# Kernel optimization log

Measured on AMD Instinct MI355X. Metric: run time of the kernel, lower is better.

The kernel has to match this reference:

```python
import jax, jax.numpy as jnp
import numpy as np

GRID_SIZE = 8
POS_LAMBDA = 250.0
POS_MARGIN = 1.0
NEG_MARGIN = 0.2


def setup_inputs() -> dict:
    key = jax.random.key(0)
    k1, k2, k3, k4 = jax.random.split(key, 4)
    N, C, Hr, Wr = 8, 128, 30, 40
    H, W = Hr * GRID_SIZE, Wr * GRID_SIZE
    des1 = jax.random.normal(k1, (N, C, Hr, Wr), jnp.float32)
    des2 = jax.random.normal(k2, (N, C, Hr, Wr), jnp.float32)
    # near-identity homography so the positive-pair mask s is non-trivial
    homo = jnp.eye(3, dtype=jnp.float32) + 0.001 * jax.random.normal(k3, (3, 3), jnp.float32)
    mask = (jax.random.uniform(k4, (N, 1, H, W)) > 0.05).astype(jnp.float32)
    return {"des1": des1, "des2": des2, "homo": homo, "mask": mask}


def reference(des1, des2, homo, mask):
    n, c, hr, wr = des1.shape
    gs = GRID_SIZE

    # coordinate grid of cell centers in full-res pixel coords: (x, y)
    ys, xs = jnp.meshgrid(jnp.arange(hr), jnp.arange(wr), indexing='ij')
    grid = jnp.stack([xs, ys], axis=-1).astype(homo.dtype) * gs + gs // 2  # Hr,Wr,2
    grid = jnp.broadcast_to(grid, (n, hr, wr, 2))

    # warp grid by homography
    gh = jnp.concatenate([grid, jnp.ones((n, hr, wr, 1), homo.dtype)], axis=-1)  # N,Hr,Wr,3
    wg = jnp.einsum('nhwk,jk->nhwj', gh, homo)
    w_grid = wg[..., :2] / wg[..., 2:3]  # N,Hr,Wr,2

    # pairwise distance between grid cells of img1 and warped cells of img2
    diff = grid[:, :, :, None, None, :] - w_grid[:, None, None, :, :, :]  # N,Hr,Wr,Hr,Wr,2
    grid_dist = jnp.sqrt(jnp.sum(diff * diff, axis=-1))                   # N,Hr,Wr,Hr,Wr
    s = (grid_dist <= gs - 0.5).astype(des1.dtype)

    # dense descriptor cross-correlation (contraction over channels)
    dot_des = jnp.einsum('ncij,nckl->nijkl', des1, des2)  # N,Hr,Wr,Hr,Wr

    pos_dist = jnp.maximum(POS_MARGIN - dot_des, 0.0)
    neg_dist = jnp.maximum(dot_des - NEG_MARGIN, 0.0)
    loss = POS_LAMBDA * s * pos_dist + (1.0 - s) * neg_dist

    # space_to_depth(mask, gs).prod(dim=1)
    m = mask.reshape(n, 1, hr, gs, wr, gs)
    r_mask = jnp.prod(m, axis=(1, 3, 5))            # N,Hr,Wr
    r_mask5 = r_mask.reshape(n, 1, 1, hr, wr)

    norm = hr * wr * jnp.sum(r_mask5)
    loss = jnp.sum(loss * r_mask5) / norm
    return (loss, s, dot_des, r_mask5[:, 0])  # r_mask squeezed -> N,1,Hr,Wr
```

## Files before the change

kernel.cpp:

```cpp
#include <hip/hip_runtime.h>
#include <hip/hip_bf16.h>

#define HRr 30
#define WRr 40
#define MM 1200
#define CC 128
#define NB 8
#define GS 8

constexpr int PT = 19;
constexpr int TILE_SH = 16 * 64 * 8;
constexpr int NTASK = 4800;

typedef __attribute__((ext_vector_type(8))) short bf16x8;
typedef __attribute__((ext_vector_type(4))) float f32x4;

__device__ inline short f2bf(float f) {
    union { float f; unsigned u; } v; v.f = f;
    unsigned r = v.u + 0x7FFFu + ((v.u >> 16) & 1u);
    return (short)(r >> 16);
}

__global__ __launch_bounds__(256) void convert_prep_kernel(const float* __restrict__ des1,
                                                           const float* __restrict__ des2,
                                                           const float* __restrict__ homo,
                                                           const float* __restrict__ mask,
                                                           short* __restrict__ wsA,
                                                           short* __restrict__ wsB,
                                                           float2* __restrict__ wgrid,
                                                           float* __restrict__ out_rmask,
                                                           float* __restrict__ ws_rmask) {
    const int t     = threadIdx.x;
    const int ptile = blockIdx.x;
    const int n     = blockIdx.z;

    if (blockIdx.y == 0) {
        const int gid = (blockIdx.z * gridDim.x + blockIdx.x) * 256 + t;
        if (gid < MM) {
            int k = gid / WRr, l = gid % WRr;
            float x = (float)(l * GS + GS / 2);
            float y = (float)(k * GS + GS / 2);
            float nx = homo[0] * x + homo[1] * y + homo[2];
            float ny = homo[3] * x + homo[4] * y + homo[5];
            float dn = homo[6] * x + homo[7] * y + homo[8];
            wgrid[gid] = make_float2(nx / dn, ny / dn);
        }
        if (gid < NB * MM) {
            int nn = gid / MM;
            int rem = gid % MM;
            int k = rem / WRr, l = rem % WRr;
            const float* mp = mask + (size_t)nn * (240 * 320) + (size_t)(k * GS) * 320 + l * GS;
            float prod = 1.f;
            #pragma unroll
            for (int yy = 0; yy < GS; ++yy) {
                float4 a = *reinterpret_cast<const float4*>(&mp[yy * 320]);
                float4 b = *reinterpret_cast<const float4*>(&mp[yy * 320 + 4]);
                prod *= a.x * a.y * a.z * a.w * b.x * b.y * b.z * b.w;
            }
            out_rmask[gid] = prod;
            ws_rmask[gid]  = prod;
        }
    }

    const int lane = t & 63;
    const int g    = t >> 6;
    const int p    = ptile * 64 + lane;
    const int kr   = blockIdx.y * 2 + (g >> 1);
    const int kb   = kr * 8;
    const int isB  = g & 1;

    const float* src = (isB ? des2 : des1) + (size_t)n * CC * MM;
    short* dst = (isB ? wsB : wsA) + (size_t)(n * PT + ptile) * TILE_SH;

    bf16x8 wv;
    #pragma unroll
    for (int i = 0; i < 8; ++i) {
        float v = (p < MM) ? src[(size_t)(kb + i) * MM + p] : 0.f;
        wv[i] = f2bf(v);
    }
    const int rb = lane >> 4, lc = lane & 15;
    const int ks = kr >> 2, lrk = kr & 3;
    const size_t off = (size_t)(((ks * 4 + rb) * 64) + lrk * 16 + lc) * 8;
    *reinterpret_cast<bf16x8*>(&dst[off]) = wv;
}

__global__ __launch_bounds__(256) void main_kernel(const short* __restrict__ wsA,
                                                   const short* __restrict__ wsB,
                                                   const float2* __restrict__ wgrid,
                                                   const float* __restrict__ rmask,
                                                   float* __restrict__ out_s,
                                                   float* __restrict__ out_dot,
                                                   float* __restrict__ partials) {
    __shared__ float Ds[16 * 164];
    __shared__ float red[4];

    const int f   = blockIdx.x;
    const int n   = f & 7;
    const int idx = f >> 3;
    const int strip  = idx >> 3;
    const int e      = idx & 7;
    const int p0     = strip * 16;
    const int fbase  = e * 9 + (e < 3 ? e : 3);
    const int nf     = (e < 3) ? 10 : 9;
    const int cbase  = fbase * 16;
    const int W      = nf * 16;

    const int t    = threadIdx.x;
    const int lane = t & 63;
    const int w    = t >> 6;
    const int lr   = lane >> 4, lc = lane & 15;

    const short* An  = wsA + (size_t)(n * PT + (p0 >> 6)) * TILE_SH;
    const int    rbA = (p0 >> 4) & 3;
    bf16x8 af[4];
    #pragma unroll
    for (int ks = 0; ks < 4; ++ks)
        af[ks] = *reinterpret_cast<const bf16x8*>(&An[(size_t)(((ks * 4 + rbA) * 64) + lane) * 8]);

    const short* Bn = wsB + (size_t)n * PT * TILE_SH;
    const float* rm = rmask + n * MM;

    for (int i = w; i < nf; i += 4) {
        const int g = fbase + i;
        const short* Bt = Bn + (size_t)(g >> 2) * TILE_SH;
        const int rbB = g & 3;
        f32x4 acc = {0.f, 0.f, 0.f, 0.f};
        #pragma unroll
        for (int ks = 0; ks < 4; ++ks) {
            bf16x8 bfr = *reinterpret_cast<const bf16x8*>(
                &Bt[(size_t)(((ks * 4 + rbB) * 64) + lane) * 8]);
            acc = __builtin_amdgcn_mfma_f32_16x16x32_bf16(af[ks], bfr, acc, 0, 0, 0);
        }
        #pragma unroll
        for (int r = 0; r < 4; ++r)
            Ds[(lr * 4 + r) * 164 + 1 + i * 16 + lc] = acc[r];
    }
    __syncthreads();

    const int row = t >> 4;
    const int l16 = t & 15;
    const int p   = p0 + row;
    const float gx = (float)((p % WRr) * GS + GS / 2);
    const float gy = (float)((p / WRr) * GS + GS / 2);
    const size_t rowbase = (size_t)(n * MM + p) * MM;
    const float* dsr = &Ds[row * 164 + 1];
    const int h = 31 - 16 * (p & 1);
    const int cAl = (((h - cbase) % 32) + 32) % 32;

    float a0 = 0.f, a1 = 0.f, a2 = 0.f, a3 = 0.f;

    for (int c = l16; c < cAl; c += 16) {
        const float dot = dsr[c];
        const int q = cbase + c;
        const float2 wg = wgrid[q];
        const float dx = gx - wg.x, dy = gy - wg.y;
        const float d2 = dx * dx + dy * dy;
        const float s = (d2 <= 56.25f) ? 1.f : 0.f;
        const float le = 250.f * s * fmaxf(1.f - dot, 0.f) + (1.f - s) * fmaxf(dot - 0.2f, 0.f);
        a0 += le * rm[q];
        out_dot[rowbase + q] = dot;
        out_s[rowbase + q] = s;
    }
    const int nl = (W - cAl) >> 5;
    const int s4 = nl << 3;
    const int ts = cAl + (nl << 5);
    for (int k = 0;; ++k) {
        const int jj = l16 + (k << 4);
        if (jj >= s4) break;
        const int c = cAl + (jj << 2);
        const int q = cbase + c;
        const f32x4 dv = *reinterpret_cast<const f32x4*>(&dsr[c]);
        f32x4 sv;
        {
            const float2 wg0 = wgrid[q];
            const float2 wg1 = wgrid[q + 1];
            const float2 wg2 = wgrid[q + 2];
            const float2 wg3 = wgrid[q + 3];
            const float dx0 = gx - wg0.x, dy0 = gy - wg0.y;
            const float dx1 = gx - wg1.x, dy1 = gy - wg1.y;
            const float dx2 = gx - wg2.x, dy2 = gy - wg2.y;
            const float dx3 = gx - wg3.x, dy3 = gy - wg3.y;
            sv[0] = (dx0 * dx0 + dy0 * dy0 <= 56.25f) ? 1.f : 0.f;
            sv[1] = (dx1 * dx1 + dy1 * dy1 <= 56.25f) ? 1.f : 0.f;
            sv[2] = (dx2 * dx2 + dy2 * dy2 <= 56.25f) ? 1.f : 0.f;
            sv[3] = (dx3 * dx3 + dy3 * dy3 <= 56.25f) ? 1.f : 0.f;
        }
        const float le0 = 250.f * sv[0] * fmaxf(1.f - dv[0], 0.f) + (1.f - sv[0]) * fmaxf(dv[0] - 0.2f, 0.f);
        const float le1 = 250.f * sv[1] * fmaxf(1.f - dv[1], 0.f) + (1.f - sv[1]) * fmaxf(dv[1] - 0.2f, 0.f);
        const float le2 = 250.f * sv[2] * fmaxf(1.f - dv[2], 0.f) + (1.f - sv[2]) * fmaxf(dv[2] - 0.2f, 0.f);
        const float le3 = 250.f * sv[3] * fmaxf(1.f - dv[3], 0.f) + (1.f - sv[3]) * fmaxf(dv[3] - 0.2f, 0.f);
        a0 += le0 * rm[q];
        a1 += le1 * rm[q + 1];
        a2 += le2 * rm[q + 2];
        a3 += le3 * rm[q + 3];
        *reinterpret_cast<f32x4*>(&out_dot[rowbase + q]) = dv;
        *reinterpret_cast<f32x4*>(&out_s[rowbase + q]) = sv;
    }
    for (int c = ts + l16; c < W; c += 16) {
        const float dot = dsr[c];
        const int q = cbase + c;
        const float2 wg = wgrid[q];
        const float dx = gx - wg.x, dy = gy - wg.y;
        const float d2 = dx * dx + dy * dy;
        const float s = (d2 <= 56.25f) ? 1.f : 0.f;
        const float le = 250.f * s * fmaxf(1.f - dot, 0.f) + (1.f - s) * fmaxf(dot - 0.2f, 0.f);
        a1 += le * rm[q];
        out_dot[rowbase + q] = dot;
        out_s[rowbase + q] = s;
    }

    float lsum = (a0 + a1) + (a2 + a3);

    #pragma unroll
    for (int off = 32; off > 0; off >>= 1)
        lsum += __shfl_xor(lsum, off, 64);
    if (lane == 0) red[w] = lsum;
    __syncthreads();
    if (t == 0)
        partials[f] = (red[0] + red[1]) + (red[2] + red[3]);
}

__global__ __launch_bounds__(1024) void final_kernel(const float* __restrict__ partials,
                                                     const float* __restrict__ rmask,
                                                     float* __restrict__ out_loss) {
    __shared__ float r1[16], r2[16];
    const int t = threadIdx.x;
    const int lane = t & 63;
    const int w = t >> 6;

    float s1 = 0.f, s2 = 0.f;
    for (int i = t; i < NTASK; i += 1024) s1 += partials[i];
    for (int i = t; i < NB * MM; i += 1024) s2 += rmask[i];
    #pragma unroll
    for (int off = 32; off > 0; off >>= 1) {
        s1 += __shfl_xor(s1, off, 64);
        s2 += __shfl_xor(s2, off, 64);
    }
    if (lane == 0) { r1[w] = s1; r2[w] = s2; }
    __syncthreads();
    if (t == 0) {
        float total = 0.f, rsum = 0.f;
        #pragma unroll
        for (int i = 0; i < 16; ++i) { total += r1[i]; rsum += r2[i]; }
        out_loss[0] = total / ((float)MM * rsum);
    }
}

extern "C" void kernel_launch(void* const* d_in, const int* in_sizes, int n_in,
                              void* d_out, int out_size, void* d_ws, size_t ws_size,
                              hipStream_t stream) {
    const float* des1 = (const float*)d_in[0];
    const float* des2 = (const float*)d_in[1];
    const float* homo = (const float*)d_in[2];
    const float* mask = (const float*)d_in[3];

    float* out      = (float*)d_out;
    float* out_loss = out;
    float* out_s    = out + 1;
    float* out_dot  = out + 1 + (size_t)NB * MM * MM;
    float* out_rm   = out + 1 + 2 * (size_t)NB * MM * MM;

    char* wsb = (char*)d_ws;
    float2* wgrid    = (float2*)(wsb);
    float*  partials = (float*)(wsb + 16384);
    float*  ws_rm    = (float*)(wsb + 65536);
    short*  wsA      = (short*)(wsb + 131072);
    short*  wsB      = wsA + (size_t)NB * PT * TILE_SH;

    dim3 cgrid(PT, 8, NB);
    convert_prep_kernel<<<cgrid, 256, 0, stream>>>(des1, des2, homo, mask,
                                                   wsA, wsB, wgrid, out_rm, ws_rm);

    main_kernel<<<dim3(NTASK, 1, 1), 256, 0, stream>>>(wsA, wsB, wgrid, ws_rm,
                                                       out_s, out_dot, partials);

    final_kernel<<<1, 1024, 0, stream>>>(partials, ws_rm, out_loss);
}
```

Before: 39.68 us.

## Make main kernel persistent with double-buffered LDS to overlap MFMA and stores

Replaces the one-tile-per-block launch of 4800 blocks with 1792 persistent blocks, each looping over tiles of its batch image. A double-buffered shared-memory tile lets the MFMA compute of the next tile run before the epilogue writes of the current one, with one barrier per iteration. This is meant to cut block launch and scheduling overhead and to overlap compute with the store-heavy epilogue. In exchange, per-block work is uneven (600 tiles over 224 blocks per image, so 2 or 3 tiles each), shared memory use doubles, and the per-block partial count changes for the final reduction.

```diff
diff --git a/kernel.cpp b/kernel.cpp
--- a/kernel.cpp
+++ b/kernel.cpp
@@ -10,7 +10,9 @@
 
 constexpr int PT = 19;
 constexpr int TILE_SH = 16 * 64 * 8;
-constexpr int NTASK = 4800;
+constexpr int NBLK = 1792;
+constexpr int BPI  = NBLK / NB;
+constexpr int TPI  = 600;
 
 typedef __attribute__((ext_vector_type(8))) short bf16x8;
 typedef __attribute__((ext_vector_type(4))) float f32x4;
@@ -91,122 +93,147 @@
                                                    float* __restrict__ out_s,
                                                    float* __restrict__ out_dot,
                                                    float* __restrict__ partials) {
-    __shared__ float Ds[16 * 164];
+    __shared__ float Ds[2][16 * 164];
     __shared__ float red[4];
 
-    const int f   = blockIdx.x;
-    const int n   = f & 7;
-    const int idx = f >> 3;
-    const int strip  = idx >> 3;
-    const int e      = idx & 7;
-    const int p0     = strip * 16;
-    const int fbase  = e * 9 + (e < 3 ? e : 3);
-    const int nf     = (e < 3) ? 10 : 9;
-    const int cbase  = fbase * 16;
-    const int W      = nf * 16;
+    const int f  = blockIdx.x;
+    const int n  = f & 7;
+    const int bi = f >> 3;
 
     const int t    = threadIdx.x;
     const int lane = t & 63;
     const int w    = t >> 6;
     const int lr   = lane >> 4, lc = lane & 15;
-
-    const short* An  = wsA + (size_t)(n * PT + (p0 >> 6)) * TILE_SH;
-    const int    rbA = (p0 >> 4) & 3;
-    bf16x8 af[4];
-    #pragma unroll
-    for (int ks = 0; ks < 4; ++ks)
-        af[ks] = *reinterpret_cast<const bf16x8*>(&An[(size_t)(((ks * 4 + rbA) * 64) + lane) * 8]);
+    const int row  = t >> 4;
+    const int l16  = t & 15;
 
     const short* Bn = wsB + (size_t)n * PT * TILE_SH;
     const float* rm = rmask + n * MM;
 
-    for (int i = w; i < nf; i += 4) {
-        const int g = fbase + i;
-        const short* Bt = Bn + (size_t)(g >> 2) * TILE_SH;
-        const int rbB = g & 3;
-        f32x4 acc = {0.f, 0.f, 0.f, 0.f};
+    float a0 = 0.f, a1 = 0.f, a2 = 0.f, a3 = 0.f;
+
+    auto compute = [&](int tt, int buf) {
+        const int strip = tt >> 3;
+        const int e     = tt & 7;
+        const int p0    = strip * 16;
+        const int fbase = e * 9 + (e < 3 ? e : 3);
+        const int nf    = (e < 3) ? 10 : 9;
+
+        const short* An  = wsA + (size_t)(n * PT + (p0 >> 6)) * TILE_SH;
+        const int    rbA = (p0 >> 4) & 3;
+        bf16x8 af[4];
         #pragma unroll
-        for (int ks = 0; ks < 4; ++ks) {
-            bf16x8 bfr = *reinterpret_cast<const bf16x8*>(
-                &Bt[(size_t)(((ks * 4 + rbB) * 64) + lane) * 8]);
-            acc = __builtin_amdgcn_mfma_f32_16x16x32_bf16(af[ks], bfr, acc, 0, 0, 0);
-        }
-        #pragma unroll
-        for (int r = 0; r < 4; ++r)
-            Ds[(lr * 4 + r) * 164 + 1 + i * 16 + lc] = acc[r];
-    }
-    __syncthreads();
-
-    const int row = t >> 4;
-    const int l16 = t & 15;
-    const int p   = p0 + row;
-    const float gx = (float)((p % WRr) * GS + GS / 2);
-    const float gy = (float)((p / WRr) * GS + GS / 2);
-    const size_t rowbase = (size_t)(n * MM + p) * MM;
-    const float* dsr = &Ds[row * 164 + 1];
-    const int h = 31 - 16 * (p & 1);
-    const int cAl = (((h - cbase) % 32) + 32) % 32;
-
-    float a0 = 0.f, a1 = 0.f, a2 = 0.f, a3 = 0.f;
-
-    for (int c = l16; c < cAl; c += 16) {
-        const float dot = dsr[c];
-        const int q = cbase + c;
-        const float2 wg = wgrid[q];
-        const float dx = gx - wg.x, dy = gy - wg.y;
-        const float d2 = dx * dx + dy * dy;
-        const float s = (d2 <= 56.25f) ? 1.f : 0.f;
-        const float le = 250.f * s * fmaxf(1.f - dot, 0.f) + (1.f - s) * fmaxf(dot - 0.2f, 0.f);
-        a0 += le * rm[q];
-        out_dot[rowbase + q] = dot;
-        out_s[rowbase + q] = s;
-    }
-    const int nl = (W - cAl) >> 5;
-    const int s4 = nl << 3;
-    const int ts = cAl + (nl << 5);
-    for (int k = 0;; ++k) {
-        const int jj = l16 + (k << 4);
-        if (jj >= s4) break;
-        const int c = cAl + (jj << 2);
-        const int q = cbase + c;
-        const f32x4 dv = *reinterpret_cast<const f32x4*>(&dsr[c]);
-        f32x4 sv;
-        {
-            const float2 wg0 = wgrid[q];
-            const float2 wg1 = wgrid[q + 1];
-            const float2 wg2 = wgrid[q + 2];
-            const float2 wg3 = wgrid[q + 3];
-            const float dx0 = gx - wg0.x, dy0 = gy - wg0.y;
-            const float dx1 = gx - wg1.x, dy1 = gy - wg1.y;
-            const float dx2 = gx - wg2.x, dy2 = gy - wg2.y;
-            const float dx3 = gx - wg3.x, dy3 = gy - wg3.y;
-            sv[0] = (dx0 * dx0 + dy0 * dy0 <= 56.25f) ? 1.f : 0.f;
-            sv[1] = (dx1 * dx1 + dy1 * dy1 <= 56.25f) ? 1.f : 0.f;
-            sv[2] = (dx2 * dx2 + dy2 * dy2 <= 56.25f) ? 1.f : 0.f;
-            sv[3] = (dx3 * dx3 + dy3 * dy3 <= 56.25f) ? 1.f : 0.f;
-        }
-        const float le0 = 250.f * sv[0] * fmaxf(1.f - dv[0], 0.f) + (1.f - sv[0]) * fmaxf(dv[0] - 0.2f, 0.f);
-        const float le1 = 250.f * sv[1] * fmaxf(1.f - dv[1], 0.f) + (1.f - sv[1]) * fmaxf(dv[1] - 0.2f, 0.f);
-        const float le2 = 250.f * sv[2] * fmaxf(1.f - dv[2], 0.f) + (1.f - sv[2]) * fmaxf(dv[2] - 0.2f, 0.f);
-        const float le3 = 250.f * sv[3] * fmaxf(1.f - dv[3], 0.f) + (1.f - sv[3]) * fmaxf(dv[3] - 0.2f, 0.f);
-        a0 += le0 * rm[q];
-        a1 += le1 * rm[q + 1];
-        a2 += le2 * rm[q + 2];
-        a3 += le3 * rm[q + 3];
-        *reinterpret_cast<f32x4*>(&out_dot[rowbase + q]) = dv;
-        *reinterpret_cast<f32x4*>(&out_s[rowbase + q]) = sv;
-    }
-    for (int c = ts + l16; c < W; c += 16) {
-        const float dot = dsr[c];
-        const int q = cbase + c;
-        const float2 wg = wgrid[q];
-        const float dx = gx - wg.x, dy = gy - wg.y;
-        const float d2 = dx * dx + dy * dy;
-        const float s = (d2 <= 56.25f) ? 1.f : 0.f;
-        const float le = 250.f * s * fmaxf(1.f - dot, 0.f) + (1.f - s) * fmaxf(dot - 0.2f, 0.f);
-        a1 += le * rm[q];
-        out_dot[rowbase + q] = dot;
-        out_s[rowbase + q] = s;
+        for (int ks = 0; ks < 4; ++ks)
+            af[ks] = *reinterpret_cast<const bf16x8*>(&An[(size_t)(((ks * 4 + rbA) * 64) + lane) * 8]);
+
+        for (int i = w; i < nf; i += 4) {
+            const int g = fbase + i;
+            const short* Bt = Bn + (size_t)(g >> 2) * TILE_SH;
+            const int rbB = g & 3;
+            f32x4 acc = {0.f, 0.f, 0.f, 0.f};
+            #pragma unroll
+            for (int ks = 0; ks < 4; ++ks) {
+                bf16x8 bfr = *reinterpret_cast<const bf16x8*>(
+                    &Bt[(size_t)(((ks * 4 + rbB) * 64) + lane) * 8]);
+                acc = __builtin_amdgcn_mfma_f32_16x16x32_bf16(af[ks], bfr, acc, 0, 0, 0);
+            }
+            #pragma unroll
+            for (int r = 0; r < 4; ++r)
+                Ds[buf][(lr * 4 + r) * 164 + 1 + i * 16 + lc] = acc[r];
+        }
+    };
+
+    auto write = [&](int tt, int buf) {
+        const int strip = tt >> 3;
+        const int e     = tt & 7;
+        const int p0    = strip * 16;
+        const int fbase = e * 9 + (e < 3 ? e : 3);
+        const int nf    = (e < 3) ? 10 : 9;
+        const int cbase = fbase * 16;
+        const int W     = nf * 16;
+
+        const int p   = p0 + row;
+        const float gx = (float)((p % WRr) * GS + GS / 2);
+        const float gy = (float)((p / WRr) * GS + GS / 2);
+        const size_t rowbase = (size_t)(n * MM + p) * MM;
+        const float* dsr = &Ds[buf][row * 164 + 1];
+        const int h = 31 - 16 * (p & 1);
+        const int cAl = (((h - cbase) % 32) + 32) % 32;
+
+        for (int c = l16; c < cAl; c += 16) {
+            const float dot = dsr[c];
+            const int q = cbase + c;
+            const float2 wg = wgrid[q];
+            const float dx = gx - wg.x, dy = gy - wg.y;
+            const float d2 = dx * dx + dy * dy;
+            const float s = (d2 <= 56.25f) ? 1.f : 0.f;
+            const float le = 250.f * s * fmaxf(1.f - dot, 0.f) + (1.f - s) * fmaxf(dot - 0.2f, 0.f);
+            a0 += le * rm[q];
+            out_dot[rowbase + q] = dot;
+            out_s[rowbase + q] = s;
+        }
+        const int nl = (W - cAl) >> 5;
+        const int s4 = nl << 3;
+        const int ts = cAl + (nl << 5);
+        for (int k = 0;; ++k) {
+            const int jj = l16 + (k << 4);
+            if (jj >= s4) break;
+            const int c = cAl + (jj << 2);
+            const int q = cbase + c;
+            const f32x4 dv = *reinterpret_cast<const f32x4*>(&dsr[c]);
+            f32x4 sv;
+            {
+                const float2 wg0 = wgrid[q];
+                const float2 wg1 = wgrid[q + 1];
+                const float2 wg2 = wgrid[q + 2];
+                const float2 wg3 = wgrid[q + 3];
+                const float dx0 = gx - wg0.x, dy0 = gy - wg0.y;
+                const float dx1 = gx - wg1.x, dy1 = gy - wg1.y;
+                const float dx2 = gx - wg2.x, dy2 = gy - wg2.y;
+                const float dx3 = gx - wg3.x, dy3 = gy - wg3.y;
+                sv[0] = (dx0 * dx0 + dy0 * dy0 <= 56.25f) ? 1.f : 0.f;
+                sv[1] = (dx1 * dx1 + dy1 * dy1 <= 56.25f) ? 1.f : 0.f;
+                sv[2] = (dx2 * dx2 + dy2 * dy2 <= 56.25f) ? 1.f : 0.f;
+                sv[3] = (dx3 * dx3 + dy3 * dy3 <= 56.25f) ? 1.f : 0.f;
+            }
+            const float le0 = 250.f * sv[0] * fmaxf(1.f - dv[0], 0.f) + (1.f - sv[0]) * fmaxf(dv[0] - 0.2f, 0.f);
+            const float le1 = 250.f * sv[1] * fmaxf(1.f - dv[1], 0.f) + (1.f - sv[1]) * fmaxf(dv[1] - 0.2f, 0.f);
+            const float le2 = 250.f * sv[2] * fmaxf(1.f - dv[2], 0.f) + (1.f - sv[2]) * fmaxf(dv[2] - 0.2f, 0.f);
+            const float le3 = 250.f * sv[3] * fmaxf(1.f - dv[3], 0.f) + (1.f - sv[3]) * fmaxf(dv[3] - 0.2f, 0.f);
+            a0 += le0 * rm[q];
+            a1 += le1 * rm[q + 1];
+            a2 += le2 * rm[q + 2];
+            a3 += le3 * rm[q + 3];
+            *reinterpret_cast<f32x4*>(&out_dot[rowbase + q]) = dv;
+            *reinterpret_cast<f32x4*>(&out_s[rowbase + q]) = sv;
+        }
+        for (int c = ts + l16; c < W; c += 16) {
+            const float dot = dsr[c];
+            const int q = cbase + c;
+            const float2 wg = wgrid[q];
+            const float dx = gx - wg.x, dy = gy - wg.y;
+            const float d2 = dx * dx + dy * dy;
+            const float s = (d2 <= 56.25f) ? 1.f : 0.f;
+            const float le = 250.f * s * fmaxf(1.f - dot, 0.f) + (1.f - s) * fmaxf(dot - 0.2f, 0.f);
+            a1 += le * rm[q];
+            out_dot[rowbase + q] = dot;
+            out_s[rowbase + q] = s;
+        }
+    };
+
+    int tt = bi;
+    if (tt < TPI) {
+        compute(tt, 0);
+        __syncthreads();
+        int cur = 0;
+        for (int tn = tt + BPI; tn < TPI; tn += BPI) {
+            compute(tn, cur ^ 1);
+            write(tt, cur);
+            __syncthreads();
+            tt = tn;
+            cur ^= 1;
+        }
+        write(tt, cur);
     }
 
     float lsum = (a0 + a1) + (a2 + a3);
@@ -229,7 +256,7 @@
     const int w = t >> 6;
 
     float s1 = 0.f, s2 = 0.f;
-    for (int i = t; i < NTASK; i += 1024) s1 += partials[i];
+    for (int i = t; i < NBLK; i += 1024) s1 += partials[i];
     for (int i = t; i < NB * MM; i += 1024) s2 += rmask[i];
     #pragma unroll
     for (int off = 32; off > 0; off >>= 1) {
@@ -271,8 +298,8 @@
     convert_prep_kernel<<<cgrid, 256, 0, stream>>>(des1, des2, homo, mask,
                                                    wsA, wsB, wgrid, out_rm, ws_rm);
 
-    main_kernel<<<dim3(NTASK, 1, 1), 256, 0, stream>>>(wsA, wsB, wgrid, ws_rm,
-                                                       out_s, out_dot, partials);
+    main_kernel<<<dim3(NBLK, 1, 1), 256, 0, stream>>>(wsA, wsB, wgrid, ws_rm,
+                                                      out_s, out_dot, partials);
 
     final_kernel<<<1, 1024, 0, stream>>>(partials, ws_rm, out_loss);
 }
```

Result: slower. 40.96 us (+3.2%).
